# Performance work log

Hardware: AMD Instinct MI355X
Metric: run time of the kernel (lower is better)

## Reference

```python
import jax, jax.numpy as jnp
import numpy as np

PADDING_BORDER = True   # padding_mode=True -> border padding
ALIGN_CORNERS = True


def setup_inputs() -> dict:
    key = jax.random.key(0)
    k1, k2 = jax.random.split(key)
    N, C, L_in, L_out = 64, 64, 4096, 8192
    inp = jax.random.normal(k1, (N, C, L_in), dtype=jnp.float32)
    grid = jax.random.uniform(k2, (N, L_out), dtype=jnp.float32) * 2.0 - 1.0  # [-1, 1]
    return {"input": inp, "grid": grid}


def _grid_sample1d(inp, grid, padding_border, align_corners):
    N, C, L = inp.shape
    # unnormalize grid coord from [-1,1] to pixel space
    if align_corners:
        x = (grid + 1.0) * 0.5 * (L - 1)
    else:
        x = ((grid + 1.0) * L - 1.0) * 0.5
    if padding_border:
        x = jnp.clip(x, 0.0, float(L - 1))
    x0 = jnp.floor(x)
    w1 = x - x0          # weight for right neighbor, [N, L_out]
    w0 = 1.0 - w1        # weight for left neighbor
    i0 = x0.astype(jnp.int32)
    i1 = i0 + 1
    if padding_border:
        m0 = jnp.ones_like(w0)
        m1 = jnp.ones_like(w1)
    else:
        m0 = ((i0 >= 0) & (i0 < L)).astype(inp.dtype)
        m1 = ((i1 >= 0) & (i1 < L)).astype(inp.dtype)
    i0c = jnp.clip(i0, 0, L - 1)
    i1c = jnp.clip(i1, 0, L - 1)
    # gather along length dim: indices broadcast over channels -> [N, C, L_out]
    v0 = jnp.take_along_axis(inp, i0c[:, None, :].repeat(1, axis=1), axis=2)
    v1 = jnp.take_along_axis(inp, i1c[:, None, :].repeat(1, axis=1), axis=2)
    out = (w0 * m0)[:, None, :] * v0 + (w1 * m1)[:, None, :] * v1
    return out


def reference(input, grid):
    return _grid_sample1d(input, grid, PADDING_BORDER, ALIGN_CORNERS)
```

## Files before the change

kernel.cpp:

```cpp
#include <hip/hip_runtime.h>


constexpr int N_    = 64;
constexpr int C_    = 64;
constexpr int L_IN  = 4096;
constexpr int L_OUT = 8192;

constexpr int BLOCK = 256;
constexpr int CPB   = 2;
constexpr int EPT   = L_OUT / BLOCK;
constexpr int NCH   = EPT / 4;
constexpr int NBLOCKS = N_ * C_ / CPB;

typedef float f32x4 __attribute__((ext_vector_type(4)));

__global__ __launch_bounds__(BLOCK, 4) void gs1d_kernel(
    const float* __restrict__ inp, const float* __restrict__ grid,
    float* __restrict__ out)
{
    __shared__ float row[CPB][L_IN];

    const int tid = threadIdx.x;
    const int bid = blockIdx.x;
    const int n   = bid >> 5;
    const int c0  = (bid & 31) * CPB;

    const float* src = inp + (size_t)(n * C_ + c0) * L_IN;
#pragma unroll
    for (int r = 0; r < CPB; ++r) {
#pragma unroll
        for (int k = 0; k < 4; ++k) {
            int e     = (k * BLOCK + tid) * 4;
            int lbase = (k * BLOCK + (tid & ~63)) * 4;
            __builtin_amdgcn_global_load_lds(
                (const __attribute__((address_space(1))) void*)(src + r * L_IN + e),
                (__attribute__((address_space(3))) void*)(&row[r][lbase]),
                16, 0, 0);
        }
    }

    const float* grow = grid + (size_t)n * L_OUT;

    int   li[EPT];
    float w1[EPT];
#pragma unroll
    for (int h = 0; h < NCH; ++h) {
        float4 g = *reinterpret_cast<const float4*>(grow + h * (BLOCK * 4) + 4 * tid);
        const float* gp = &g.x;
#pragma unroll
        for (int j = 0; j < 4; ++j) {
            float x = (gp[j] + 1.0f) * 0.5f * (float)(L_IN - 1);
            x = fminf(fmaxf(x, 0.0f), (float)(L_IN - 1));
            float xf = floorf(x);
            int   i0 = (int)xf;
            float w  = x - xf;
            li[h * 4 + j] = min(i0, L_IN - 2);
            w1[h * 4 + j] = (i0 >= L_IN - 1) ? 1.0f : w;
        }
    }

    __syncthreads();

    float* orow = out + (size_t)(n * C_ + c0) * L_OUT;

#pragma unroll
    for (int h = 0; h < NCH; ++h) {
        f32x4 o0, o1;
#pragma unroll
        for (int j = 0; j < 4; ++j) {
            int   p  = h * 4 + j;
            float a0 = row[0][li[p]];
            float b0 = row[0][li[p] + 1];
            float a1 = row[1][li[p]];
            float b1 = row[1][li[p] + 1];
            o0[j] = fmaf(w1[p], b0 - a0, a0);
            o1[j] = fmaf(w1[p], b1 - a1, a1);
        }
        __builtin_nontemporal_store(o0,
            reinterpret_cast<f32x4*>(orow + h * (BLOCK * 4) + 4 * tid));
        __builtin_nontemporal_store(o1,
            reinterpret_cast<f32x4*>(orow + L_OUT + h * (BLOCK * 4) + 4 * tid));
    }
}

extern "C" void kernel_launch(void* const* d_in, const int* in_sizes, int n_in,
                              void* d_out, int out_size, void* d_ws, size_t ws_size,
                              hipStream_t stream) {
    const float* inp  = (const float*)d_in[0];
    const float* grid = (const float*)d_in[1];
    float* out = (float*)d_out;
    gs1d_kernel<<<NBLOCKS, BLOCK, 0, stream>>>(inp, grid, out);
}
```

Measured before the change: 179.6 us.

## Double-buffer LDS channel rows across multiple channel pairs per block

```diff
diff --git a/kernel.cpp b/kernel.cpp
--- a/kernel.cpp
+++ b/kernel.cpp
@@ -8,36 +8,44 @@
 
 constexpr int BLOCK = 256;
 constexpr int CPB   = 2;
+constexpr int T     = 4;
 constexpr int EPT   = L_OUT / BLOCK;
 constexpr int NCH   = EPT / 4;
-constexpr int NBLOCKS = N_ * C_ / CPB;
+constexpr int KSTEP = L_IN / (BLOCK * 4);
+constexpr int LPT   = CPB * KSTEP;
+constexpr int NBLOCKS = N_ * C_ / (CPB * T);
 
 typedef float f32x4 __attribute__((ext_vector_type(4)));
 
-__global__ __launch_bounds__(BLOCK, 4) void gs1d_kernel(
+__global__ __launch_bounds__(BLOCK, 2) void gs1d_kernel(
     const float* __restrict__ inp, const float* __restrict__ grid,
     float* __restrict__ out)
 {
-    __shared__ float row[CPB][L_IN];
+    __shared__ float buf[2][CPB][L_IN];
 
     const int tid = threadIdx.x;
     const int bid = blockIdx.x;
-    const int n   = bid >> 5;
-    const int c0  = (bid & 31) * CPB;
+    const int n   = bid >> 3;
+    const int g   = bid & 7;
 
-    const float* src = inp + (size_t)(n * C_ + c0) * L_IN;
+    const float* src0 = inp + ((size_t)n * C_ + (size_t)g * (CPB * T)) * L_IN;
+
+    auto stage = [&](int bsel, int t) {
+        const float* s = src0 + (size_t)t * CPB * L_IN;
 #pragma unroll
-    for (int r = 0; r < CPB; ++r) {
+        for (int r = 0; r < CPB; ++r)
 #pragma unroll
-        for (int k = 0; k < 4; ++k) {
-            int e     = (k * BLOCK + tid) * 4;
-            int lbase = (k * BLOCK + (tid & ~63)) * 4;
-            __builtin_amdgcn_global_load_lds(
-                (const __attribute__((address_space(1))) void*)(src + r * L_IN + e),
-                (__attribute__((address_space(3))) void*)(&row[r][lbase]),
-                16, 0, 0);
-        }
-    }
+            for (int k = 0; k < KSTEP; ++k) {
+                int e     = (k * BLOCK + tid) * 4;
+                int lbase = (k * BLOCK + (tid & ~63)) * 4;
+                __builtin_amdgcn_global_load_lds(
+                    (const __attribute__((address_space(1))) void*)(s + r * L_IN + e),
+                    (__attribute__((address_space(3))) void*)(&buf[bsel][r][lbase]),
+                    16, 0, 0);
+            }
+    };
+
+    stage(0, 0);
 
     const float* grow = grid + (size_t)n * L_OUT;
 
@@ -45,8 +53,8 @@
     float w1[EPT];
 #pragma unroll
     for (int h = 0; h < NCH; ++h) {
-        float4 g = *reinterpret_cast<const float4*>(grow + h * (BLOCK * 4) + 4 * tid);
-        const float* gp = &g.x;
+        float4 gv = *reinterpret_cast<const float4*>(grow + h * (BLOCK * 4) + 4 * tid);
+        const float* gp = &gv.x;
 #pragma unroll
         for (int j = 0; j < 4; ++j) {
             float x = (gp[j] + 1.0f) * 0.5f * (float)(L_IN - 1);
@@ -59,27 +67,47 @@
         }
     }
 
-    __syncthreads();
-
-    float* orow = out + (size_t)(n * C_ + c0) * L_OUT;
+    float* obase = out + ((size_t)n * C_ + (size_t)g * (CPB * T)) * L_OUT;
 
 #pragma unroll
-    for (int h = 0; h < NCH; ++h) {
-        f32x4 o0, o1;
+    for (int t = 0; t < T; ++t) {
+        if (t + 1 < T) {
+            stage((t + 1) & 1, t + 1);
+            asm volatile("s_waitcnt vmcnt(8)" ::: "memory");
+        } else {
+            asm volatile("s_waitcnt vmcnt(0)" ::: "memory");
+        }
+        __builtin_amdgcn_s_barrier();
+        __builtin_amdgcn_sched_barrier(0);
+
+        const float* r0 = &buf[t & 1][0][0];
+        const float* r1 = &buf[t & 1][1][0];
+        float* orow = obase + (size_t)t * CPB * L_OUT;
+
 #pragma unroll
-        for (int j = 0; j < 4; ++j) {
-            int   p  = h * 4 + j;
-            float a0 = row[0][li[p]];
-            float b0 = row[0][li[p] + 1];
-            float a1 = row[1][li[p]];
-            float b1 = row[1][li[p] + 1];
-            o0[j] = fmaf(w1[p], b0 - a0, a0);
-            o1[j] = fmaf(w1[p], b1 - a1, a1);
+        for (int h = 0; h < NCH; ++h) {
+            f32x4 o0, o1;
+#pragma unroll
+            for (int j = 0; j < 4; ++j) {
+                int   p  = h * 4 + j;
+                int   q  = li[p];
+                float a0 = r0[q];
+                float b0 = r0[q + 1];
+                float a1 = r1[q];
+                float b1 = r1[q + 1];
+                o0[j] = fmaf(w1[p], b0 - a0, a0);
+                o1[j] = fmaf(w1[p], b1 - a1, a1);
+            }
+            __builtin_nontemporal_store(o0,
+                reinterpret_cast<f32x4*>(orow + h * (BLOCK * 4) + 4 * tid));
+            __builtin_nontemporal_store(o1,
+                reinterpret_cast<f32x4*>(orow + L_OUT + h * (BLOCK * 4) + 4 * tid));
         }
-        __builtin_nontemporal_store(o0,
-            reinterpret_cast<f32x4*>(orow + h * (BLOCK * 4) + 4 * tid));
-        __builtin_nontemporal_store(o1,
-            reinterpret_cast<f32x4*>(orow + L_OUT + h * (BLOCK * 4) + 4 * tid));
+
+        if (t + 1 < T) {
+            __builtin_amdgcn_sched_barrier(0);
+            __builtin_amdgcn_s_barrier();
+        }
     }
 }
 
```

New measurement: 187.9 us. 4.6% more time.
